# Kernel tuning notes

Hardware: AMD Instinct MI355X
Metric: run time of the kernel (lower is better)

The kernel has to match this reference:

```python
import jax, jax.numpy as jnp
import numpy as np

# Static hyperparameters matching init_kwargs
G, N, D = 8, 8, 8          # groups, filters/group, kernel depth (c = G*D, o = G*N)
W, KS = 16, 4              # kernel width (time window), time stride
AH, AS = 2, 2              # activate_height, activate_stride (freq box-sum window)
C, F = 64, 128             # input channels, embedding (freq bins)
O = G * N                  # out_channels


def setup_inputs() -> dict:
    key = jax.random.key(0)
    kx, kw = jax.random.split(key)
    x = jax.random.normal(kx, (16, C, F, 256), dtype=jnp.float32)
    # xavier-uniform for weight (o, d, e, w)
    fan_in = D * F * W
    fan_out = fan_in  # torch xavier on 4D: fan computed over receptive field; bound below matches scale
    bound = float(np.sqrt(6.0 / (fan_in + fan_out)))
    weight = jax.random.uniform(kw, (O, D, F, W), dtype=jnp.float32, minval=-bound, maxval=bound)
    return {"x": x, "weight": weight}


def reference(x, weight):
    b, c, f, T = x.shape
    t = (T - W) // KS + 1
    # unfold time: x[..., ti*KS + wi] -> [b, c, f, t, W]
    idx = jnp.arange(t)[:, None] * KS + jnp.arange(W)[None, :]
    xu = x[..., idx]
    # split channels (g d) row-major, matching einops 'b (g d) f t w'
    xg = xu.reshape(b, G, D, f, t, W)
    wg = weight.reshape(G, N, D, f, W)
    # fused: multiply-broadcast then sum over d and w (the ones-kernel conv sums
    # over depth d and full width w); height window handled below.
    z = jnp.einsum('bgdftw,gndfw->btgnf', xg, wg)  # [b, t, G, N, f]
    z = z.reshape(b, t, O, f)
    # box-sum over freq with window AH, stride AS ('valid')
    fp = (f - AH) // AS + 1
    pidx = jnp.arange(fp)[:, None] * AS + jnp.arange(AH)
    y = z[..., pidx].sum(-1)  # [b, t, O, fp]
    return jnp.transpose(y, (0, 2, 3, 1))  # [b, O, fp, t]
```

## Files before the change

kernel.cpp:

```cpp
#include <hip/hip_runtime.h>


namespace {
constexpr int kB  = 16;
constexpr int kC  = 64;
constexpr int kF  = 128;
constexpr int kT  = 256;
constexpr int kG  = 8;
constexpr int kD  = 8;
constexpr int kN  = 8;
constexpr int kW  = 16;
constexpr int kKS = 4;
constexpr int kNT = 61;
constexpr int kO  = 64;
constexpr int kFP = 64;
constexpr int kWStride = kD * kF * kW;
}

__global__ __launch_bounds__(256, 3)
void lc2d_kernel(const float* __restrict__ x,
                 const float* __restrict__ wt,
                 float* __restrict__ out) {
  __shared__ float4 wlds[512];

  const int tid  = threadIdx.x;
  const int lane = tid & 63;
  const int wq   = tid >> 6;
  const int tl   = lane & 31;
  const int th   = lane >> 5;
  const int fi   = blockIdx.x;
  const int g    = blockIdx.y;
  const int tz   = blockIdx.z;

  {
    const float* wb = wt + ((size_t)(g * kN) * kD * kF + (size_t)fi * 2) * kW;
#pragma unroll
    for (int r = 0; r < 2; ++r) {
      const int q  = tid + r * 256;
      const int n  = q >> 6;
      const int dd = (q >> 3) & 7;
      const int fr = (q >> 2) & 1;
      const int qq = q & 3;
      const float* src =
          wb + (size_t)n * kWStride + dd * (kF * kW) + fr * kW + qq * 4;
      wlds[q] = *(const float4*)src;
    }
  }

  const int tg = tz * 32 + tl;
  const int tc = (tg < kNT) ? tl : (kNT - 1 - 32);
  const int tau0 = (tz * 32 + tc) * kKS + th * 8;

  const float* xb[4];
#pragma unroll
  for (int bb = 0; bb < 4; ++bb) {
    const int b = wq * 4 + bb;
    xb[bb] = x + (((size_t)b * kC + g * kD) * kF + fi * 2) * kT + tau0;
  }

  float acc[4][kN];
#pragma unroll
  for (int bb = 0; bb < 4; ++bb)
#pragma unroll
    for (int n = 0; n < kN; ++n) acc[bb][n] = 0.f;

  float4 cur[4][2];
#pragma unroll
  for (int bb = 0; bb < 4; ++bb)
#pragma unroll
    for (int q = 0; q < 2; ++q) cur[bb][q] = ((const float4*)xb[bb])[q];

  __syncthreads();

#pragma unroll 2
  for (int it = 0; it < 16; ++it) {
    const int nx = (it < 15) ? it + 1 : 15;
    const size_t roff = ((size_t)(nx >> 1) * kF + (nx & 1)) * kT;
    float4 pre[4][2];
#pragma unroll
    for (int bb = 0; bb < 4; ++bb) {
      const float* xr = xb[bb] + roff;
#pragma unroll
      for (int q = 0; q < 2; ++q) pre[bb][q] = ((const float4*)xr)[q];
    }

    const float4* wrow = &wlds[it * 4 + th * 2];
#pragma unroll
    for (int n = 0; n < kN; ++n) {
      const float4 w0 = wrow[n * 64];
      const float4 w1 = wrow[n * 64 + 1];
#pragma unroll
      for (int bb = 0; bb < 4; ++bb) {
        float a = acc[bb][n];
        a = fmaf(cur[bb][0].x, w0.x, a);
        a = fmaf(cur[bb][0].y, w0.y, a);
        a = fmaf(cur[bb][0].z, w0.z, a);
        a = fmaf(cur[bb][0].w, w0.w, a);
        a = fmaf(cur[bb][1].x, w1.x, a);
        a = fmaf(cur[bb][1].y, w1.y, a);
        a = fmaf(cur[bb][1].z, w1.z, a);
        a = fmaf(cur[bb][1].w, w1.w, a);
        acc[bb][n] = a;
      }
    }

#pragma unroll
    for (int bb = 0; bb < 4; ++bb)
#pragma unroll
      for (int q = 0; q < 2; ++q) cur[bb][q] = pre[bb][q];
  }

#pragma unroll
  for (int bb = 0; bb < 4; ++bb)
#pragma unroll
    for (int n = 0; n < kN; ++n)
      acc[bb][n] += __shfl_xor(acc[bb][n], 32);

  if (tg < kNT) {
    const size_t s = (size_t)kFP * kNT;
    const int nb = th * 4;
#pragma unroll
    for (int bb = 0; bb < 4; ++bb) {
      const int b = wq * 4 + bb;
      float* ob =
          out + (((size_t)b * kO + g * kN + nb) * kFP + fi) * (size_t)kNT + tg;
#pragma unroll
      for (int j = 0; j < 4; ++j) ob[(size_t)j * s] = acc[bb][nb + j];
    }
  }
}

extern "C" void kernel_launch(void* const* d_in, const int* in_sizes, int n_in,
                              void* d_out, int out_size, void* d_ws, size_t ws_size,
                              hipStream_t stream) {
  const float* x  = (const float*)d_in[0];
  const float* wt = (const float*)d_in[1];
  float* out      = (float*)d_out;

  dim3 grid(kFP, kG, 2);
  lc2d_kernel<<<grid, 256, 0, stream>>>(x, wt, out);
}
```

Before: 231.4 us.

## Stage x rows in LDS via direct global-to-LDS loads, one wave per timeline

```diff
diff --git a/kernel.cpp b/kernel.cpp
--- a/kernel.cpp
+++ b/kernel.cpp
@@ -1,36 +1,40 @@
 #include <hip/hip_runtime.h>
+#include <stdint.h>
 
 
 namespace {
-constexpr int kB  = 16;
 constexpr int kC  = 64;
 constexpr int kF  = 128;
 constexpr int kT  = 256;
-constexpr int kG  = 8;
 constexpr int kD  = 8;
 constexpr int kN  = 8;
 constexpr int kW  = 16;
-constexpr int kKS = 4;
 constexpr int kNT = 61;
 constexpr int kO  = 64;
 constexpr int kFP = 64;
 constexpr int kWStride = kD * kF * kW;
 }
 
-__global__ __launch_bounds__(256, 3)
+typedef float f32x4 __attribute__((ext_vector_type(4)));
+
+__device__ __forceinline__ void gload_lds16(const float* gsrc, float* ldsdst) {
+  __builtin_amdgcn_global_load_lds(
+      (const __attribute__((address_space(1))) uint32_t*)gsrc,
+      (__attribute__((address_space(3))) uint32_t*)ldsdst, 16, 0, 0);
+}
+
+__global__ __launch_bounds__(256, 2)
 void lc2d_kernel(const float* __restrict__ x,
                  const float* __restrict__ wt,
                  float* __restrict__ out) {
-  __shared__ float4 wlds[512];
+  __shared__ f32x4 wlds[512];
+  __shared__ f32x4 xlds[2][16][64];
 
   const int tid  = threadIdx.x;
   const int lane = tid & 63;
   const int wq   = tid >> 6;
-  const int tl   = lane & 31;
-  const int th   = lane >> 5;
   const int fi   = blockIdx.x;
   const int g    = blockIdx.y;
-  const int tz   = blockIdx.z;
 
   {
     const float* wb = wt + ((size_t)(g * kN) * kD * kF + (size_t)fi * 2) * kW;
@@ -41,22 +45,28 @@
       const int dd = (q >> 3) & 7;
       const int fr = (q >> 2) & 1;
       const int qq = q & 3;
-      const float* src =
-          wb + (size_t)n * kWStride + dd * (kF * kW) + fr * kW + qq * 4;
-      wlds[q] = *(const float4*)src;
+      wlds[q] = *(const f32x4*)(wb + (size_t)n * kWStride + dd * (kF * kW) +
+                                fr * kW + qq * 4);
     }
   }
 
-  const int tg = tz * 32 + tl;
-  const int tc = (tg < kNT) ? tl : (kNT - 1 - 32);
-  const int tau0 = (tz * 32 + tc) * kKS + th * 8;
-
-  const float* xb[4];
+  const float* xrow[4];
 #pragma unroll
   for (int bb = 0; bb < 4; ++bb) {
     const int b = wq * 4 + bb;
-    xb[bb] = x + (((size_t)b * kC + g * kD) * kF + fi * 2) * kT + tau0;
+    xrow[bb] = x + ((size_t)(b * kC + g * kD) * kF + fi * 2) * kT;
   }
+
+  const int pinv = (lane & 56) | ((lane - (lane >> 3)) & 7);
+
+  const int tcl = (lane < kNT) ? lane : (kNT - 1);
+  int pj[4];
+#pragma unroll
+  for (int j = 0; j < 4; ++j) {
+    const int q = tcl + j;
+    pj[j] = ((q & 56) | ((q + (q >> 3)) & 7)) << 4;
+  }
+  const char* xbase = (const char*)&xlds[0][0][0];
 
   float acc[4][kN];
 #pragma unroll
@@ -64,68 +74,72 @@
 #pragma unroll
     for (int n = 0; n < kN; ++n) acc[bb][n] = 0.f;
 
-  float4 cur[4][2];
 #pragma unroll
   for (int bb = 0; bb < 4; ++bb)
+    gload_lds16(xrow[bb] + 4 * pinv, (float*)&xlds[0][wq * 4 + bb][0]);
+
+  int cur = 0;
+  for (int it = 0; it < 16; ++it) {
+    __syncthreads();
+
+    if (it < 15) {
+      const int nx = it + 1;
+      const int roff = (nx >> 1) * (kF * kT) + (nx & 1) * kT;
 #pragma unroll
-    for (int q = 0; q < 2; ++q) cur[bb][q] = ((const float4*)xb[bb])[q];
+      for (int bb = 0; bb < 4; ++bb)
+        gload_lds16(xrow[bb] + roff + 4 * pinv,
+                    (float*)&xlds[cur ^ 1][wq * 4 + bb][0]);
+    }
 
-  __syncthreads();
-
-#pragma unroll 2
-  for (int it = 0; it < 16; ++it) {
-    const int nx = (it < 15) ? it + 1 : 15;
-    const size_t roff = ((size_t)(nx >> 1) * kF + (nx & 1)) * kT;
-    float4 pre[4][2];
+    const int qb = it * 4;
+    f32x4 xq[4][4];
 #pragma unroll
     for (int bb = 0; bb < 4; ++bb) {
-      const float* xr = xb[bb] + roff;
+      const char* rb = xbase + cur * 16384 + (wq * 4 + bb) * 1024;
 #pragma unroll
-      for (int q = 0; q < 2; ++q) pre[bb][q] = ((const float4*)xr)[q];
+      for (int j = 0; j < 4; ++j)
+        xq[bb][j] = *(const f32x4*)(rb + pj[j]);
     }
-
-    const float4* wrow = &wlds[it * 4 + th * 2];
 #pragma unroll
     for (int n = 0; n < kN; ++n) {
-      const float4 w0 = wrow[n * 64];
-      const float4 w1 = wrow[n * 64 + 1];
+      const f32x4 w0 = wlds[n * 64 + qb + 0];
+      const f32x4 w1 = wlds[n * 64 + qb + 1];
+      const f32x4 w2 = wlds[n * 64 + qb + 2];
+      const f32x4 w3 = wlds[n * 64 + qb + 3];
 #pragma unroll
       for (int bb = 0; bb < 4; ++bb) {
         float a = acc[bb][n];
-        a = fmaf(cur[bb][0].x, w0.x, a);
-        a = fmaf(cur[bb][0].y, w0.y, a);
-        a = fmaf(cur[bb][0].z, w0.z, a);
-        a = fmaf(cur[bb][0].w, w0.w, a);
-        a = fmaf(cur[bb][1].x, w1.x, a);
-        a = fmaf(cur[bb][1].y, w1.y, a);
-        a = fmaf(cur[bb][1].z, w1.z, a);
-        a = fmaf(cur[bb][1].w, w1.w, a);
+        a = fmaf(xq[bb][0].x, w0.x, a);
+        a = fmaf(xq[bb][0].y, w0.y, a);
+        a = fmaf(xq[bb][0].z, w0.z, a);
+        a = fmaf(xq[bb][0].w, w0.w, a);
+        a = fmaf(xq[bb][1].x, w1.x, a);
+        a = fmaf(xq[bb][1].y, w1.y, a);
+        a = fmaf(xq[bb][1].z, w1.z, a);
+        a = fmaf(xq[bb][1].w, w1.w, a);
+        a = fmaf(xq[bb][2].x, w2.x, a);
+        a = fmaf(xq[bb][2].y, w2.y, a);
+        a = fmaf(xq[bb][2].z, w2.z, a);
+        a = fmaf(xq[bb][2].w, w2.w, a);
+        a = fmaf(xq[bb][3].x, w3.x, a);
+        a = fmaf(xq[bb][3].y, w3.y, a);
+        a = fmaf(xq[bb][3].z, w3.z, a);
+        a = fmaf(xq[bb][3].w, w3.w, a);
         acc[bb][n] = a;
       }
     }
-
-#pragma unroll
-    for (int bb = 0; bb < 4; ++bb)
-#pragma unroll
-      for (int q = 0; q < 2; ++q) cur[bb][q] = pre[bb][q];
+    cur ^= 1;
   }
 
-#pragma unroll
-  for (int bb = 0; bb < 4; ++bb)
-#pragma unroll
-    for (int n = 0; n < kN; ++n)
-      acc[bb][n] += __shfl_xor(acc[bb][n], 32);
-
-  if (tg < kNT) {
+  if (lane < kNT) {
     const size_t s = (size_t)kFP * kNT;
-    const int nb = th * 4;
 #pragma unroll
     for (int bb = 0; bb < 4; ++bb) {
       const int b = wq * 4 + bb;
       float* ob =
-          out + (((size_t)b * kO + g * kN + nb) * kFP + fi) * (size_t)kNT + tg;
+          out + (((size_t)b * kO + g * kN) * kFP + fi) * (size_t)kNT + lane;
 #pragma unroll
-      for (int j = 0; j < 4; ++j) ob[(size_t)j * s] = acc[bb][nb + j];
+      for (int n = 0; n < kN; ++n) ob[(size_t)n * s] = acc[bb][n];
     }
   }
 }
@@ -137,6 +151,6 @@
   const float* wt = (const float*)d_in[1];
   float* out      = (float*)d_out;
 
-  dim3 grid(kFP, kG, 2);
+  dim3 grid(kFP, 8, 1);
   lc2d_kernel<<<grid, 256, 0, stream>>>(x, wt, out);
 }
```

After: 197.8 us. 14.5% less time.
